# Kernel tuning notes

Measured on AMD Instinct MI355X. Metric: run time of the kernel, lower is better.

The kernel has to match this reference:

```python
import jax, jax.numpy as jnp
import numpy as np
from jax import lax

DG, KH, KW = 8, 3, 3
STRIDE, PAD, DIL = 1, 1, 1


def setup_inputs() -> dict:
    key = jax.random.key(0)
    ks = jax.random.split(key, 6)
    B, C, H, W = 4, 256, 64, 64
    Cout = 256
    off_ch = DG * 3 * KH * KW  # 216
    x = jax.random.normal(ks[0], (B, C, H, W), dtype=jnp.float32)
    extra_feat = jax.random.normal(ks[1], (B, C, H, W), dtype=jnp.float32)
    weight = jax.random.normal(ks[2], (Cout, C, KH, KW), dtype=jnp.float32) * 0.02
    bias = jax.random.normal(ks[3], (Cout,), dtype=jnp.float32) * 0.01
    off_w = jax.random.normal(ks[4], (off_ch, C, KH, KW), dtype=jnp.float32) * 0.01
    off_b = jax.random.normal(ks[5], (off_ch,), dtype=jnp.float32) * 0.01
    return {"x": x, "extra_feat": extra_feat, "weight": weight, "bias": bias,
            "off_w": off_w, "off_b": off_b}


def _modulated_deform_conv(x, offset, mask, weight, bias):
    B, C, H, W = x.shape
    Cout = weight.shape[0]
    K = KH * KW
    Ho, Wo = offset.shape[2], offset.shape[3]
    Cg = C // DG

    # offset: [B, 2*DG*K, Ho, Wo] interpreted as (dg, K, (dy, dx)) interleaved
    off = offset.reshape(B, DG, K, 2, Ho, Wo)
    dy, dx = off[:, :, :, 0], off[:, :, :, 1]  # [B, DG, K, Ho, Wo]

    ky = jnp.repeat(jnp.arange(KH), KW)  # [K]
    kx = jnp.tile(jnp.arange(KW), KH)    # [K]
    base_y = (jnp.arange(Ho) * STRIDE - PAD)[None, None, None, :, None] + (ky * DIL)[None, None, :, None, None]
    base_x = (jnp.arange(Wo) * STRIDE - PAD)[None, None, None, None, :] + (kx * DIL)[None, None, :, None, None]
    py = dy + base_y  # [B, DG, K, Ho, Wo]
    px = dx + base_x

    y0f = jnp.floor(py)
    x0f = jnp.floor(px)
    fy = py - y0f
    fx = px - x0f
    y0 = y0f.astype(jnp.int32)
    x0 = x0f.astype(jnp.int32)

    xg = x.reshape(B, DG, Cg, H * W)
    N = K * Ho * Wo

    def gather(yi, xi):
        valid = ((yi >= 0) & (yi < H) & (xi >= 0) & (xi < W)).astype(x.dtype)
        idx = (jnp.clip(yi, 0, H - 1) * W + jnp.clip(xi, 0, W - 1)).reshape(B, DG, 1, N)
        g = jnp.take_along_axis(xg, jnp.broadcast_to(idx, (B, DG, Cg, N)), axis=-1)
        g = g.reshape(B, DG, Cg, K, Ho, Wo)
        return g * valid[:, :, None]

    val = (((1 - fy) * (1 - fx))[:, :, None] * gather(y0, x0)
           + ((1 - fy) * fx)[:, :, None] * gather(y0, x0 + 1)
           + (fy * (1 - fx))[:, :, None] * gather(y0 + 1, x0)
           + (fy * fx)[:, :, None] * gather(y0 + 1, x0 + 1))
    val = val * mask.reshape(B, DG, 1, K, Ho, Wo)
    val = val.reshape(B, C, K, Ho, Wo)

    out = jnp.einsum('bckhw,ock->bohw', val, weight.reshape(Cout, C, K))
    return out + bias[None, :, None, None]


def reference(x, extra_feat, weight, bias, off_w, off_b):
    # conv_offset: plain conv predicting offsets + mask
    om = lax.conv_general_dilated(
        extra_feat, off_w, window_strides=(STRIDE, STRIDE),
        padding=((PAD, PAD), (PAD, PAD)), rhs_dilation=(DIL, DIL),
        dimension_numbers=('NCHW', 'OIHW', 'NCHW')) + off_b[None, :, None, None]
    o1, o2, mask = jnp.split(om, 3, axis=1)
    offset = jnp.concatenate([o1, o2], axis=1)
    mask = jax.nn.sigmoid(mask)
    return _modulated_deform_conv(x, offset, mask, weight, bias)
```

## Files before the change

### kernel.cpp

```cpp
#include <hip/hip_runtime.h>
#include <hip/hip_bf16.h>
#include <math.h>

#define BB 4
#define CC 256
#define HH 64
#define WW 64
#define HW 4096
#define PH 68
#define PW 68
#define COUT 256
#define OFFC 216
#define KTOT 2304
#define NCHUNK 72

typedef __attribute__((ext_vector_type(4))) float f32x4;
typedef __attribute__((ext_vector_type(8))) short s16x8;
typedef __attribute__((ext_vector_type(8))) unsigned short u16x8;
typedef __attribute__((ext_vector_type(2))) unsigned int u32x2;

__device__ __forceinline__ unsigned short f2bf(float f) {
    unsigned int u = __float_as_uint(f);
    return (unsigned short)((u + 0x7fffu + ((u >> 16) & 1u)) >> 16);
}
__device__ __forceinline__ float bflo(unsigned int u) { return __uint_as_float(u << 16); }
__device__ __forceinline__ float bfhi(unsigned int u) { return __uint_as_float(u & 0xffff0000u); }
__device__ __forceinline__ unsigned int pkbf(float a, float b) {
    __hip_bfloat162 h = __float22bfloat162_rn(make_float2(a, b));
    unsigned int r;
    __builtin_memcpy(&r, &h, 4);
    return r;
}

#define WAITL() asm volatile("s_waitcnt lgkmcnt(0)" ::: "memory")
#define RBAR() __builtin_amdgcn_s_barrier()

__global__ __launch_bounds__(256) void pack_w_both(const float* __restrict__ wmain,
                                                   const float* __restrict__ woff,
                                                   unsigned short* __restrict__ wpm,
                                                   unsigned short* __restrict__ wpo) {
    int idx = blockIdx.x * 256 + threadIdx.x;
    int t = idx >> 13, r = idx & 8191;
    int oc = r >> 5, s = (r >> 3) & 3, e = r & 7;
    int kk = ((s ^ ((oc >> 1) & 3)) << 3) | e;
    if (blockIdx.y == 0) {
        int dg = t / 9, tap = t - dg * 9;
        int c = dg * 32 + kk;
        wpm[idx] = f2bf(wmain[((size_t)oc * CC + c) * 9 + tap]);
    } else {
        int tap = t >> 3, cg = t & 7;
        int c = cg * 32 + kk;
        float v = (oc < OFFC) ? woff[((size_t)oc * CC + c) * 9 + tap] : 0.f;
        wpo[idx] = f2bf(v);
    }
}

__global__ __launch_bounds__(256) void pad_tr2(const float* __restrict__ srcx,
                                               const float* __restrict__ srce,
                                               unsigned short* __restrict__ dx_,
                                               unsigned short* __restrict__ de_) {
    const float* src = blockIdx.y ? srce : srcx;
    unsigned short* dst = blockIdx.y ? de_ : dx_;
    int blk = blockIdx.x;
    int b = blk / PH, yp = blk % PH;
    int y = yp - 2;
    unsigned short* drow = dst + ((size_t)b * PH + yp) * PW * CC;
    int tid = threadIdx.x;
    if ((unsigned)y >= (unsigned)HH) {
        for (int i = tid; i < PW * CC / 8; i += 256) *(u16x8*)&drow[(size_t)i * 8] = (u16x8)0;
        return;
    }
    __shared__ float tile[64][65];
    int lane = tid & 63, w = tid >> 6;
    int oct = tid & 7, xi = tid >> 3;
    const float* srow = src + (size_t)b * CC * HW + (size_t)y * WW;
    for (int chunk = 0; chunk < 4; chunk++) {
        __syncthreads();
#pragma unroll
        for (int i = 0; i < 16; i++) {
            int c = chunk * 64 + w * 16 + i;
            tile[w * 16 + i][lane] = srow[(size_t)c * HW + lane];
        }
        __syncthreads();
#pragma unroll
        for (int xq = 0; xq < 3; xq++) {
            int xp = xq * 32 + xi;
            if (xp < PW) {
                int x = xp - 2;
                u16x8 v = (u16x8)0;
                if ((unsigned)x < (unsigned)WW) {
#pragma unroll
                    for (int e = 0; e < 8; e++) v[e] = f2bf(tile[oct * 8 + e][x]);
                }
                *(u16x8*)&drow[(size_t)xp * CC + chunk * 64 + oct * 8] = v;
            }
        }
    }
}


#define A_LOAD(WPP, T, AF)                                                \
    {                                                                     \
        const unsigned short* wt_ = WPP + (size_t)(T) * 8192 + aoff;      \
        AF[0] = *(const s16x8*)&wt_[0];                                   \
        AF[1] = *(const s16x8*)&wt_[512];                                 \
        AF[2] = *(const s16x8*)&wt_[8192];                                \
        AF[3] = *(const s16x8*)&wt_[8704];                                \
    }

#define MFMA8R(AC, BUF)                                                                      \
    {                                                                                        \
        int sw_ = (lg ^ ((r16 >> 1) & 3)) << 3;                                              \
        s16x8 b0_ = *(const s16x8*)&sB[BUF][0][r16 * 32 + sw_];                              \
        s16x8 b1_ = *(const s16x8*)&sB[BUF][0][(16 + r16) * 32 + sw_];                       \
        s16x8 b2_ = *(const s16x8*)&sB[BUF][1][r16 * 32 + sw_];                              \
        s16x8 b3_ = *(const s16x8*)&sB[BUF][1][(16 + r16) * 32 + sw_];                       \
        __builtin_amdgcn_s_setprio(1);                                                       \
        acc[0][0] = __builtin_amdgcn_mfma_f32_16x16x32_bf16(AC[0], b0_, acc[0][0], 0, 0, 0); \
        acc[0][1] = __builtin_amdgcn_mfma_f32_16x16x32_bf16(AC[0], b1_, acc[0][1], 0, 0, 0); \
        acc[1][0] = __builtin_amdgcn_mfma_f32_16x16x32_bf16(AC[1], b0_, acc[1][0], 0, 0, 0); \
        acc[1][1] = __builtin_amdgcn_mfma_f32_16x16x32_bf16(AC[1], b1_, acc[1][1], 0, 0, 0); \
        acc[0][0] = __builtin_amdgcn_mfma_f32_16x16x32_bf16(AC[2], b2_, acc[0][0], 0, 0, 0); \
        acc[0][1] = __builtin_amdgcn_mfma_f32_16x16x32_bf16(AC[2], b3_, acc[0][1], 0, 0, 0); \
        acc[1][0] = __builtin_amdgcn_mfma_f32_16x16x32_bf16(AC[3], b2_, acc[1][0], 0, 0, 0); \
        acc[1][1] = __builtin_amdgcn_mfma_f32_16x16x32_bf16(AC[3], b3_, acc[1][1], 0, 0, 0); \
        __builtin_amdgcn_s_setprio(0);                                                       \
    }

__global__ __launch_bounds__(512, 4) void fused_dcn(const unsigned short* __restrict__ eT,
                                                    const unsigned short* __restrict__ xT,
                                                    const unsigned short* __restrict__ wpo,
                                                    const unsigned short* __restrict__ wpm,
                                                    const float* __restrict__ off_b,
                                                    const float* __restrict__ bias,
                                                    float* __restrict__ out) {
    __shared__ __align__(16) unsigned short sB[2][2][1024];
    __shared__ __align__(16) unsigned int prep[NCHUNK][32][3];
    __shared__ float sAcc[OFFC * 33];

    int bxl = (blockIdx.x & 7) * 32 + (blockIdx.x >> 3);
    int b = bxl >> 6, y = bxl & 63;
    int pxh = blockIdx.y;
    int tid = threadIdx.x;
    int lane = tid & 63;
    int w = tid >> 6;
    int r16 = lane & 15, lg = lane >> 4;
    int aoff = (w * 32 + r16) * 32 + ((lg ^ ((r16 >> 1) & 3)) << 3);
    int p1px = tid >> 4, ch2 = tid & 15;
    int pxg = pxh * 32 + p1px;
    int kt = tid >> 8;
    int p2px = (tid >> 3) & 31;
    int ch4 = tid & 7;

    const unsigned short* eb = eT + (size_t)b * PH * PW * CC;
    const unsigned short* xb = xT + (size_t)b * PH * PW * CC;

    f32x4 acc[2][2];
#pragma unroll
    for (int mi = 0; mi < 2; mi++)
#pragma unroll
        for (int ni = 0; ni < 2; ni++) acc[mi][ni] = (f32x4)0.f;

    s16x8 aA[4], aB[4];

#define BSLOT2 (p1px * 32 + ((((ch2 >> 2) ^ ((p1px >> 1) & 3))) << 3) + (ch2 & 3) * 2)
#define OF_B(T, BV)                                                                          \
    {                                                                                        \
        int tap_ = (T) >> 3, cg_ = (T) & 7;                                                  \
        int ky_ = tap_ / 3, kx_ = tap_ - ky_ * 3;                                            \
        BV = *(const unsigned int*)&eb[(size_t)((y + ky_ + 1) * PW + (pxg + kx_ + 1)) * CC + \
                                       cg_ * 32 + ch2 * 2];                                  \
    }
#define OF_ITF(T, BUF, AC, AN, BP0, BP1, BN0, BN1)               \
    {                                                            \
        A_LOAD(wpo, (T) + 2, AN)                                 \
        OF_B((T) + 4, BN0)                                       \
        OF_B((T) + 5, BN1)                                       \
        MFMA8R(AC, BUF)                                          \
        *(unsigned int*)&sB[(BUF) ^ 1][0][BSLOT2] = BP0;         \
        *(unsigned int*)&sB[(BUF) ^ 1][1][BSLOT2] = BP1;         \
        WAITL();                                                 \
        RBAR();                                                  \
    }

    {
        unsigned int bP0, bP1, bN0, bN1;
        {
            A_LOAD(wpo, 0, aA)
            unsigned int c0, c1;
            OF_B(0, c0)
            OF_B(1, c1)
            *(unsigned int*)&sB[0][0][BSLOT2] = c0;
            *(unsigned int*)&sB[0][1][BSLOT2] = c1;
            OF_B(2, bP0)
            OF_B(3, bP1)
            WAITL();
            RBAR();
        }
        for (int t = 0; t < 68; t += 4) {
            OF_ITF(t, 0, aA, aB, bP0, bP1, bN0, bN1)
            OF_ITF(t + 2, 1, aB, aA, bN0, bN1, bP0, bP1)
        }
        {
            A_LOAD(wpo, 70, aB)
            MFMA8R(aA, 0)
            *(unsigned int*)&sB[1][0][BSLOT2] = bP0;
            *(unsigned int*)&sB[1][1][BSLOT2] = bP1;
            WAITL();
            RBAR();
        }
        MFMA8R(aB, 1)
    }

    __syncthreads();
#pragma unroll
    for (int mi = 0; mi < 2; mi++) {
#pragma unroll
        for (int ni = 0; ni < 2; ni++) {
#pragma unroll
            for (int j = 0; j < 4; j++) {
                int oc = w * 32 + mi * 16 + lg * 4 + j;
                if (oc < OFFC) sAcc[oc * 33 + ni * 16 + r16] = acc[mi][ni][j] + off_b[oc];
            }
        }
    }
    __syncthreads();
    for (int i = tid; i < NCHUNK * 32; i += 512) {
        int tt = i >> 5, px = i & 31;
        int dg = (tt * 57) >> 9;
        int tap = tt - dg * 9;
        int ky = tap / 3, kx = tap - ky * 3;
        float dyv = sAcc[(dg * 18 + 2 * tap) * 33 + px];
        float dxv = sAcc[(dg * 18 + 2 * tap + 1) * 33 + px];
        float mr = sAcc[(144 + dg * 9 + tap) * 33 + px];
        int xg = pxh * 32 + px;
        float mv = 1.f / (1.f + __expf(-mr));
        float py = (float)(y + ky - 1) + dyv;
        float pxx = (float)(xg + kx - 1) + dxv;
        float y0f = floorf(py), x0f = floorf(pxx);
        float fy = py - y0f, fx = pxx - x0f;
        int yp0 = min(max((int)y0f + 2, 0), PH - 1);
        int yp1 = min(max((int)y0f + 3, 0), PH - 1);
        int xp0 = min(max((int)x0f + 2, 0), PW - 1);
        int xp1 = min(max((int)x0f + 3, 0), PW - 1);
        prep[tt][px][0] = (unsigned int)(yp0 * PW + xp0) | ((unsigned int)(xp1 - xp0) << 13) |
                          ((unsigned int)(yp1 - yp0) << 14);
        float w00 = (1.f - fy) * (1.f - fx) * mv;
        float w01 = (1.f - fy) * fx * mv;
        float w10 = fy * (1.f - fx) * mv;
        float w11 = fy * fx * mv;
        prep[tt][px][1] = pkbf(w00, w01);
        prep[tt][px][2] = pkbf(w10, w11);
    }
    __syncthreads();

#pragma unroll
    for (int mi = 0; mi < 2; mi++)
#pragma unroll
        for (int ni = 0; ni < 2; ni++) acc[mi][ni] = (f32x4)0.f;

#define BSLOT4 (p2px * 32 + ((((ch4 >> 1) ^ ((p2px >> 1) & 3))) << 3) + (ch4 & 1) * 4)
#define DC_G(T, G00, G01, G10, G11)                                       \
    {                                                                     \
        int dg_ = ((T) * 57) >> 9;                                        \
        unsigned int iv_ = prep[T][p2px][0];                              \
        int o00_ = (int)(iv_ & 8191u) << 8;                               \
        int dxe_ = (int)((iv_ >> 13) & 1u) << 8;                          \
        int dye_ = ((iv_ >> 14) & 1u) ? (PW * CC) : 0;                    \
        const unsigned short* p_ = xb + dg_ * 32 + ch4 * 4;               \
        G00 = *(const u32x2*)(p_ + o00_);                                 \
        G01 = *(const u32x2*)(p_ + o00_ + dxe_);                          \
        G10 = *(const u32x2*)(p_ + o00_ + dye_);                          \
        G11 = *(const u32x2*)(p_ + o00_ + dye_ + dxe_);                   \
    }
#define DC_FIN(T, G00, G01, G10, G11, BUF)                                                \
    {                                                                                     \
        unsigned int wa_ = prep[T][p2px][1];                                              \
        unsigned int wb_ = prep[T][p2px][2];                                              \
        float w00 = bflo(wa_), w01 = bfhi(wa_);                                           \
        float w10 = bflo(wb_), w11 = bfhi(wb_);                                           \
        float v0 = w00 * bflo(G00[0]) + w01 * bflo(G01[0]) + w10 * bflo(G10[0]) +         \
                   w11 * bflo(G11[0]);                                                    \
        float v1 = w00 * bfhi(G00[0]) + w01 * bfhi(G01[0]) + w10 * bfhi(G10[0]) +         \
                   w11 * bfhi(G11[0]);                                                    \
        float v2 = w00 * bflo(G00[1]) + w01 * bflo(G01[1]) + w10 * bflo(G10[1]) +         \
                   w11 * bflo(G11[1]);                                                    \
        float v3 = w00 * bfhi(G00[1]) + w01 * bfhi(G01[1]) + w10 * bfhi(G10[1]) +         \
                   w11 * bfhi(G11[1]);                                                    \
        u32x2 pk_;                                                                        \
        pk_[0] = pkbf(v0, v1);                                                            \
        pk_[1] = pkbf(v2, v3);                                                            \
        *(u32x2*)&sB[BUF][kt][BSLOT4] = pk_;                                              \
    }
#define DC_ITF(T, BUF, AC, AN, GP0, GP1, GP2, GP3, GN0, GN1, GN2, GN3)     \
    {                                                                      \
        A_LOAD(wpm, (T) + 2, AN)                                           \
        DC_G((T) + 4 + kt, GN0, GN1, GN2, GN3)                             \
        MFMA8R(AC, BUF)                                                    \
        DC_FIN((T) + 2 + kt, GP0, GP1, GP2, GP3, (BUF) ^ 1)                \
        WAITL();                                                           \
        RBAR();                                                            \
    }

    {
        u32x2 gA0, gA1, gA2, gA3, gB0, gB1, gB2, gB3;
        {
            A_LOAD(wpm, 0, aA)
            u32x2 t0, t1, t2, t3;
            DC_G(kt, t0, t1, t2, t3)
            DC_FIN(kt, t0, t1, t2, t3, 0)
            DC_G(2 + kt, gA0, gA1, gA2, gA3)
            WAITL();
            RBAR();
        }
        for (int t = 0; t < 64; t += 4) {
            DC_ITF(t, 0, aA, aB, gA0, gA1, gA2, gA3, gB0, gB1, gB2, gB3)
            DC_ITF(t + 2, 1, aB, aA, gB0, gB1, gB2, gB3, gA0, gA1, gA2, gA3)
        }
        DC_ITF(64, 0, aA, aB, gA0, gA1, gA2, gA3, gB0, gB1, gB2, gB3)
        DC_ITF(66, 1, aB, aA, gB0, gB1, gB2, gB3, gA0, gA1, gA2, gA3)
        {
            A_LOAD(wpm, 70, aB)
            MFMA8R(aA, 0)
            DC_FIN(70 + kt, gA0, gA1, gA2, gA3, 1)
            WAITL();
            RBAR();
        }
        MFMA8R(aB, 1)
    }

#pragma unroll
    for (int mi = 0; mi < 2; mi++) {
#pragma unroll
        for (int ni = 0; ni < 2; ni++) {
#pragma unroll
            for (int j = 0; j < 4; j++) {
                int oc = w * 32 + mi * 16 + lg * 4 + j;
                int pxo = pxh * 32 + ni * 16 + r16;
                out[(size_t)(b * COUT + oc) * HW + y * WW + pxo] = acc[mi][ni][j] + bias[oc];
            }
        }
    }
}

extern "C" void kernel_launch(void* const* d_in, const int* in_sizes, int n_in,
                              void* d_out, int out_size, void* d_ws, size_t ws_size,
                              hipStream_t stream) {
    const float* x = (const float*)d_in[0];
    const float* extra_feat = (const float*)d_in[1];
    const float* weight = (const float*)d_in[2];
    const float* bias = (const float*)d_in[3];
    const float* off_w = (const float*)d_in[4];
    const float* off_b = (const float*)d_in[5];
    float* out = (float*)d_out;

    unsigned short* wpm = (unsigned short*)d_ws;
    unsigned short* wpo = wpm + (size_t)KTOT * COUT;
    unsigned short* xT = wpo + (size_t)KTOT * COUT;
    unsigned short* eT = xT + (size_t)BB * PH * PW * CC;

    pack_w_both<<<dim3((KTOT * COUT) / 256, 2), 256, 0, stream>>>(weight, off_w, wpm, wpo);
    pad_tr2<<<dim3(BB * PH, 2), 256, 0, stream>>>(x, extra_feat, xT, eT);

    fused_dcn<<<dim3(BB * HH, 2), 512, 0, stream>>>(eT, xT, wpo, wpm, off_b, bias, out);
}
```

Before: 89.34 us.

## Retile fused DCN to 16-pixel blocks with 4 waves each covering 64 channels

Changes the block from 512 threads covering 32 output pixels to 256 threads covering 16 pixels, with a doubled grid in the pixel dimension. Each wave now computes 64 output channels by 16 pixels using four accumulators and eight A fragments. This raises the number of blocks and shrinks shared memory per block, which should improve occupancy and load balance across CUs. The cost is that weight (A) fragments are reloaded twice as often per pixel, since each block reuses them over fewer pixels. Register pressure per thread also goes up, and the s_setprio hints around the MFMA sequence are removed.

```diff
diff --git a/kernel.cpp b/kernel.cpp
--- a/kernel.cpp
+++ b/kernel.cpp
@@ -104,108 +104,100 @@
         const unsigned short* wt_ = WPP + (size_t)(T) * 8192 + aoff;      \
         AF[0] = *(const s16x8*)&wt_[0];                                   \
         AF[1] = *(const s16x8*)&wt_[512];                                 \
-        AF[2] = *(const s16x8*)&wt_[8192];                                \
-        AF[3] = *(const s16x8*)&wt_[8704];                                \
+        AF[2] = *(const s16x8*)&wt_[1024];                                \
+        AF[3] = *(const s16x8*)&wt_[1536];                                \
+        AF[4] = *(const s16x8*)&wt_[8192];                                \
+        AF[5] = *(const s16x8*)&wt_[8704];                                \
+        AF[6] = *(const s16x8*)&wt_[9216];                                \
+        AF[7] = *(const s16x8*)&wt_[9728];                                \
     }
 
 #define MFMA8R(AC, BUF)                                                                      \
     {                                                                                        \
         int sw_ = (lg ^ ((r16 >> 1) & 3)) << 3;                                              \
         s16x8 b0_ = *(const s16x8*)&sB[BUF][0][r16 * 32 + sw_];                              \
-        s16x8 b1_ = *(const s16x8*)&sB[BUF][0][(16 + r16) * 32 + sw_];                       \
-        s16x8 b2_ = *(const s16x8*)&sB[BUF][1][r16 * 32 + sw_];                              \
-        s16x8 b3_ = *(const s16x8*)&sB[BUF][1][(16 + r16) * 32 + sw_];                       \
-        __builtin_amdgcn_s_setprio(1);                                                       \
-        acc[0][0] = __builtin_amdgcn_mfma_f32_16x16x32_bf16(AC[0], b0_, acc[0][0], 0, 0, 0); \
-        acc[0][1] = __builtin_amdgcn_mfma_f32_16x16x32_bf16(AC[0], b1_, acc[0][1], 0, 0, 0); \
-        acc[1][0] = __builtin_amdgcn_mfma_f32_16x16x32_bf16(AC[1], b0_, acc[1][0], 0, 0, 0); \
-        acc[1][1] = __builtin_amdgcn_mfma_f32_16x16x32_bf16(AC[1], b1_, acc[1][1], 0, 0, 0); \
-        acc[0][0] = __builtin_amdgcn_mfma_f32_16x16x32_bf16(AC[2], b2_, acc[0][0], 0, 0, 0); \
-        acc[0][1] = __builtin_amdgcn_mfma_f32_16x16x32_bf16(AC[2], b3_, acc[0][1], 0, 0, 0); \
-        acc[1][0] = __builtin_amdgcn_mfma_f32_16x16x32_bf16(AC[3], b2_, acc[1][0], 0, 0, 0); \
-        acc[1][1] = __builtin_amdgcn_mfma_f32_16x16x32_bf16(AC[3], b3_, acc[1][1], 0, 0, 0); \
-        __builtin_amdgcn_s_setprio(0);                                                       \
-    }
-
-__global__ __launch_bounds__(512, 4) void fused_dcn(const unsigned short* __restrict__ eT,
+        s16x8 b1_ = *(const s16x8*)&sB[BUF][1][r16 * 32 + sw_];                              \
+        acc[0] = __builtin_amdgcn_mfma_f32_16x16x32_bf16(AC[0], b0_, acc[0], 0, 0, 0);       \
+        acc[1] = __builtin_amdgcn_mfma_f32_16x16x32_bf16(AC[1], b0_, acc[1], 0, 0, 0);       \
+        acc[2] = __builtin_amdgcn_mfma_f32_16x16x32_bf16(AC[2], b0_, acc[2], 0, 0, 0);       \
+        acc[3] = __builtin_amdgcn_mfma_f32_16x16x32_bf16(AC[3], b0_, acc[3], 0, 0, 0);       \
+        acc[0] = __builtin_amdgcn_mfma_f32_16x16x32_bf16(AC[4], b1_, acc[0], 0, 0, 0);       \
+        acc[1] = __builtin_amdgcn_mfma_f32_16x16x32_bf16(AC[5], b1_, acc[1], 0, 0, 0);       \
+        acc[2] = __builtin_amdgcn_mfma_f32_16x16x32_bf16(AC[6], b1_, acc[2], 0, 0, 0);       \
+        acc[3] = __builtin_amdgcn_mfma_f32_16x16x32_bf16(AC[7], b1_, acc[3], 0, 0, 0);       \
+    }
+
+#define BSLOT (spx * 32 + (((ch4 >> 1) ^ ((spx >> 1) & 3)) << 3) + (ch4 & 1) * 4)
+
+__global__ __launch_bounds__(256, 4) void fused_dcn(const unsigned short* __restrict__ eT,
                                                     const unsigned short* __restrict__ xT,
                                                     const unsigned short* __restrict__ wpo,
                                                     const unsigned short* __restrict__ wpm,
                                                     const float* __restrict__ off_b,
                                                     const float* __restrict__ bias,
                                                     float* __restrict__ out) {
-    __shared__ __align__(16) unsigned short sB[2][2][1024];
-    __shared__ __align__(16) unsigned int prep[NCHUNK][32][3];
-    __shared__ float sAcc[OFFC * 33];
+    __shared__ __align__(16) unsigned short sB[2][2][512];
+    __shared__ __align__(16) unsigned int prep[NCHUNK][16][3];
+    __shared__ float sAcc[OFFC * 17];
 
     int bxl = (blockIdx.x & 7) * 32 + (blockIdx.x >> 3);
     int b = bxl >> 6, y = bxl & 63;
-    int pxh = blockIdx.y;
+    int pxq = blockIdx.y;
     int tid = threadIdx.x;
     int lane = tid & 63;
     int w = tid >> 6;
     int r16 = lane & 15, lg = lane >> 4;
-    int aoff = (w * 32 + r16) * 32 + ((lg ^ ((r16 >> 1) & 3)) << 3);
-    int p1px = tid >> 4, ch2 = tid & 15;
-    int pxg = pxh * 32 + p1px;
-    int kt = tid >> 8;
-    int p2px = (tid >> 3) & 31;
+    int aoff = (w * 64 + r16) * 32 + ((lg ^ ((r16 >> 1) & 3)) << 3);
+    int kt = tid >> 7;
+    int spx = (tid >> 3) & 15;
     int ch4 = tid & 7;
+    int pxg = pxq * 16 + spx;
 
     const unsigned short* eb = eT + (size_t)b * PH * PW * CC;
     const unsigned short* xb = xT + (size_t)b * PH * PW * CC;
 
-    f32x4 acc[2][2];
-#pragma unroll
-    for (int mi = 0; mi < 2; mi++)
-#pragma unroll
-        for (int ni = 0; ni < 2; ni++) acc[mi][ni] = (f32x4)0.f;
-
-    s16x8 aA[4], aB[4];
-
-#define BSLOT2 (p1px * 32 + ((((ch2 >> 2) ^ ((p1px >> 1) & 3))) << 3) + (ch2 & 3) * 2)
-#define OF_B(T, BV)                                                                          \
-    {                                                                                        \
-        int tap_ = (T) >> 3, cg_ = (T) & 7;                                                  \
-        int ky_ = tap_ / 3, kx_ = tap_ - ky_ * 3;                                            \
-        BV = *(const unsigned int*)&eb[(size_t)((y + ky_ + 1) * PW + (pxg + kx_ + 1)) * CC + \
-                                       cg_ * 32 + ch2 * 2];                                  \
-    }
-#define OF_ITF(T, BUF, AC, AN, BP0, BP1, BN0, BN1)               \
+    f32x4 acc[4];
+#pragma unroll
+    for (int mi = 0; mi < 4; mi++) acc[mi] = (f32x4)0.f;
+
+    s16x8 aA[8], aB[8];
+
+#define OF_B(T, BV)                                                                         \
+    {                                                                                       \
+        int tap_ = (T) >> 3, cg_ = (T) & 7;                                                 \
+        int ky_ = tap_ / 3, kx_ = tap_ - ky_ * 3;                                           \
+        BV = *(const u32x2*)&eb[(size_t)((y + ky_ + 1) * PW + (pxg + kx_ + 1)) * CC +       \
+                                cg_ * 32 + ch4 * 4];                                        \
+    }
+#define OF_ITF(T, BUF, AC, AN, BP, BN)                           \
     {                                                            \
         A_LOAD(wpo, (T) + 2, AN)                                 \
-        OF_B((T) + 4, BN0)                                       \
-        OF_B((T) + 5, BN1)                                       \
+        OF_B((T) + 4 + kt, BN)                                   \
         MFMA8R(AC, BUF)                                          \
-        *(unsigned int*)&sB[(BUF) ^ 1][0][BSLOT2] = BP0;         \
-        *(unsigned int*)&sB[(BUF) ^ 1][1][BSLOT2] = BP1;         \
+        *(u32x2*)&sB[(BUF) ^ 1][kt][BSLOT] = BP;                 \
         WAITL();                                                 \
         RBAR();                                                  \
     }
 
     {
-        unsigned int bP0, bP1, bN0, bN1;
+        u32x2 bP, bN;
         {
             A_LOAD(wpo, 0, aA)
-            unsigned int c0, c1;
-            OF_B(0, c0)
-            OF_B(1, c1)
-            *(unsigned int*)&sB[0][0][BSLOT2] = c0;
-            *(unsigned int*)&sB[0][1][BSLOT2] = c1;
-            OF_B(2, bP0)
-            OF_B(3, bP1)
+            u32x2 c0;
+            OF_B(kt, c0)
+            *(u32x2*)&sB[0][kt][BSLOT] = c0;
+            OF_B(2 + kt, bP)
             WAITL();
             RBAR();
         }
         for (int t = 0; t < 68; t += 4) {
-            OF_ITF(t, 0, aA, aB, bP0, bP1, bN0, bN1)
-            OF_ITF(t + 2, 1, aB, aA, bN0, bN1, bP0, bP1)
+            OF_ITF(t, 0, aA, aB, bP, bN)
+            OF_ITF(t + 2, 1, aB, aA, bN, bP)
         }
         {
             A_LOAD(wpo, 70, aB)
             MFMA8R(aA, 0)
-            *(unsigned int*)&sB[1][0][BSLOT2] = bP0;
-            *(unsigned int*)&sB[1][1][BSLOT2] = bP1;
+            *(u32x2*)&sB[1][kt][BSLOT] = bP;
             WAITL();
             RBAR();
         }
@@ -214,26 +206,23 @@
 
     __syncthreads();
 #pragma unroll
-    for (int mi = 0; mi < 2; mi++) {
-#pragma unroll
-        for (int ni = 0; ni < 2; ni++) {
-#pragma unroll
-            for (int j = 0; j < 4; j++) {
-                int oc = w * 32 + mi * 16 + lg * 4 + j;
-                if (oc < OFFC) sAcc[oc * 33 + ni * 16 + r16] = acc[mi][ni][j] + off_b[oc];
-            }
+    for (int mi = 0; mi < 4; mi++) {
+#pragma unroll
+        for (int j = 0; j < 4; j++) {
+            int oc = w * 64 + mi * 16 + lg * 4 + j;
+            if (oc < OFFC) sAcc[oc * 17 + r16] = acc[mi][j] + off_b[oc];
         }
     }
     __syncthreads();
-    for (int i = tid; i < NCHUNK * 32; i += 512) {
-        int tt = i >> 5, px = i & 31;
+    for (int i = tid; i < NCHUNK * 16; i += 256) {
+        int tt = i >> 4, px = i & 15;
         int dg = (tt * 57) >> 9;
         int tap = tt - dg * 9;
         int ky = tap / 3, kx = tap - ky * 3;
-        float dyv = sAcc[(dg * 18 + 2 * tap) * 33 + px];
-        float dxv = sAcc[(dg * 18 + 2 * tap + 1) * 33 + px];
-        float mr = sAcc[(144 + dg * 9 + tap) * 33 + px];
-        int xg = pxh * 32 + px;
+        float dyv = sAcc[(dg * 18 + 2 * tap) * 17 + px];
+        float dxv = sAcc[(dg * 18 + 2 * tap + 1) * 17 + px];
+        float mr = sAcc[(144 + dg * 9 + tap) * 17 + px];
+        int xg = pxq * 16 + px;
         float mv = 1.f / (1.f + __expf(-mr));
         float py = (float)(y + ky - 1) + dyv;
         float pxx = (float)(xg + kx - 1) + dxv;
@@ -255,15 +244,12 @@
     __syncthreads();
 
 #pragma unroll
-    for (int mi = 0; mi < 2; mi++)
-#pragma unroll
-        for (int ni = 0; ni < 2; ni++) acc[mi][ni] = (f32x4)0.f;
-
-#define BSLOT4 (p2px * 32 + ((((ch4 >> 1) ^ ((p2px >> 1) & 3))) << 3) + (ch4 & 1) * 4)
+    for (int mi = 0; mi < 4; mi++) acc[mi] = (f32x4)0.f;
+
 #define DC_G(T, G00, G01, G10, G11)                                       \
     {                                                                     \
         int dg_ = ((T) * 57) >> 9;                                        \
-        unsigned int iv_ = prep[T][p2px][0];                              \
+        unsigned int iv_ = prep[T][spx][0];                               \
         int o00_ = (int)(iv_ & 8191u) << 8;                               \
         int dxe_ = (int)((iv_ >> 13) & 1u) << 8;                          \
         int dye_ = ((iv_ >> 14) & 1u) ? (PW * CC) : 0;                    \
@@ -275,8 +261,8 @@
     }
 #define DC_FIN(T, G00, G01, G10, G11, BUF)                                                \
     {                                                                                     \
-        unsigned int wa_ = prep[T][p2px][1];                                              \
-        unsigned int wb_ = prep[T][p2px][2];                                              \
+        unsigned int wa_ = prep[T][spx][1];                                               \
+        unsigned int wb_ = prep[T][spx][2];                                               \
         float w00 = bflo(wa_), w01 = bfhi(wa_);                                           \
         float w10 = bflo(wb_), w11 = bfhi(wb_);                                           \
         float v0 = w00 * bflo(G00[0]) + w01 * bflo(G01[0]) + w10 * bflo(G10[0]) +         \
@@ -290,7 +276,7 @@
         u32x2 pk_;                                                                        \
         pk_[0] = pkbf(v0, v1);                                                            \
         pk_[1] = pkbf(v2, v3);                                                            \
-        *(u32x2*)&sB[BUF][kt][BSLOT4] = pk_;                                              \
+        *(u32x2*)&sB[BUF][kt][BSLOT] = pk_;                                               \
     }
 #define DC_ITF(T, BUF, AC, AN, GP0, GP1, GP2, GP3, GN0, GN1, GN2, GN3)     \
     {                                                                      \
@@ -330,15 +316,12 @@
     }
 
 #pragma unroll
-    for (int mi = 0; mi < 2; mi++) {
-#pragma unroll
-        for (int ni = 0; ni < 2; ni++) {
-#pragma unroll
-            for (int j = 0; j < 4; j++) {
-                int oc = w * 32 + mi * 16 + lg * 4 + j;
-                int pxo = pxh * 32 + ni * 16 + r16;
-                out[(size_t)(b * COUT + oc) * HW + y * WW + pxo] = acc[mi][ni][j] + bias[oc];
-            }
+    for (int mi = 0; mi < 4; mi++) {
+#pragma unroll
+        for (int j = 0; j < 4; j++) {
+            int oc = w * 64 + mi * 16 + lg * 4 + j;
+            int pxo = pxq * 16 + r16;
+            out[(size_t)(b * COUT + oc) * HW + y * WW + pxo] = acc[mi][j] + bias[oc];
         }
     }
 }
@@ -362,5 +345,5 @@
     pack_w_both<<<dim3((KTOT * COUT) / 256, 2), 256, 0, stream>>>(weight, off_w, wpm, wpo);
     pad_tr2<<<dim3(BB * PH, 2), 256, 0, stream>>>(x, extra_feat, xT, eT);
 
-    fused_dcn<<<dim3(BB * HH, 2), 512, 0, stream>>>(eT, xT, wpo, wpm, off_b, bias, out);
-}
+    fused_dcn<<<dim3(BB * HH, 4), 256, 0, stream>>>(eT, xT, wpo, wpm, off_b, bias, out);
+}
```

Result: slower. 130.7 us (+46.3%).
